# Kernel optimization log

Hardware: AMD Instinct MI355X
Metric: run time of the kernel (lower is better)

The kernel has to match this reference:

```python
import jax, jax.numpy as jnp
from jax import lax
import numpy as np

B, T, D, H = 2048, 512, 16, 48


def _lstm_layer(x, W_ih, W_hh, b_ih, b_hh):
    """Single-layer LSTM, batch_first. x: [B,T,Din] -> hs: [B,T,H].
    PyTorch gate order: i, f, g, o."""
    h_dim = W_hh.shape[1]
    # Precompute input contribution for all timesteps: [B,T,4H]
    xg = jnp.einsum('btd,gd->btg', x, W_ih) + b_ih + b_hh
    xg = jnp.swapaxes(xg, 0, 1)  # [T,B,4H]

    def step(carry, xg_t):
        h, c = carry
        gates = xg_t + h @ W_hh.T  # [B,4H]
        i, f, g, o = jnp.split(gates, 4, axis=-1)
        i = jax.nn.sigmoid(i)
        f = jax.nn.sigmoid(f)
        g = jnp.tanh(g)
        o = jax.nn.sigmoid(o)
        c = f * c + i * g
        h = o * jnp.tanh(c)
        return (h, c), h

    bsz = x.shape[0]
    init = (jnp.zeros((bsz, h_dim), x.dtype), jnp.zeros((bsz, h_dim), x.dtype))
    _, hs = lax.scan(step, init, xg)
    return jnp.swapaxes(hs, 0, 1)  # [B,T,H]


def setup_inputs() -> dict:
    key = jax.random.key(0)
    ks = jax.random.split(key, 11)
    s_in = 1.0 / np.sqrt(H)
    return {
        'x': jax.random.normal(ks[0], (B, T, D), jnp.float32),
        'W_ih0': jax.random.normal(ks[1], (4 * H, D), jnp.float32) * s_in,
        'W_hh0': jax.random.normal(ks[2], (4 * H, H), jnp.float32) * s_in,
        'b_ih0': jax.random.normal(ks[3], (4 * H,), jnp.float32) * s_in,
        'b_hh0': jax.random.normal(ks[4], (4 * H,), jnp.float32) * s_in,
        'W_ih1': jax.random.normal(ks[5], (4 * H, H), jnp.float32) * s_in,
        'W_hh1': jax.random.normal(ks[6], (4 * H, H), jnp.float32) * s_in,
        'b_ih1': jax.random.normal(ks[7], (4 * H,), jnp.float32) * s_in,
        'b_hh1': jax.random.normal(ks[8], (4 * H,), jnp.float32) * s_in,
        'fc_w': jax.random.normal(ks[9], (1, H), jnp.float32) * s_in,
        'fc_b': jax.random.normal(ks[10], (1,), jnp.float32) * s_in,
    }


def reference(x, W_ih0, W_hh0, b_ih0, b_hh0, W_ih1, W_hh1, b_ih1, b_hh1, fc_w, fc_b):
    # 2-layer LSTM (eval mode: inter-layer dropout is identity)
    h1 = _lstm_layer(x, W_ih0, W_hh0, b_ih0, b_hh0)   # [B,T,H]
    h2 = _lstm_layer(h1, W_ih1, W_hh1, b_ih1, b_hh1)  # [B,T,H]
    last = h2[:, -1, :]                               # [B,H]
    logits = last @ fc_w.T + fc_b                     # [B,1]
    return jax.nn.sigmoid(logits)
```

## Files before the change

kernel.cpp:

```cpp
#include <hip/hip_runtime.h>

#define TT 512
#define DD 16
#define HH 48
#define BT 8
#define NTHR 768
#define CHUNK 64

#define XA0H 16384
#define XA1  17920
#define STOT 20992

typedef short bf8v __attribute__((ext_vector_type(8)));
typedef float f32x4 __attribute__((ext_vector_type(4)));

__device__ __forceinline__ ushort bfb(float f) {
    return __builtin_bit_cast(ushort, (__bf16)f);
}

__device__ __forceinline__ float actf(float x, float A, float M, float Bc) {
    float e = __builtin_amdgcn_exp2f(M * x);
    return __builtin_fmaf(A, __builtin_amdgcn_rcpf(1.0f + e), Bc);
}

__device__ __forceinline__ void barrier_lds() {
    asm volatile("s_waitcnt lgkmcnt(0)\ns_barrier" ::: "memory");
}

__global__ __launch_bounds__(NTHR)
void lstm_kernel(const float* __restrict__ x,
                 const float* __restrict__ Wih0, const float* __restrict__ Whh0,
                 const float* __restrict__ bih0, const float* __restrict__ bhh0,
                 const float* __restrict__ Wih1, const float* __restrict__ Whh1,
                 const float* __restrict__ bih1, const float* __restrict__ bhh1,
                 const float* __restrict__ fcw, const float* __restrict__ fcb,
                 float* __restrict__ out)
{
    __shared__ alignas(16) ushort S[STOT];
    __shared__ float outl[BT][HH];

    const int tid  = threadIdx.x;
    const int lane = tid & 63;
    const int wave = tid >> 6;
    const int b0   = blockIdx.x * BT;

    const int colq = lane & 15;
    const int quad = lane >> 4;
    const int u    = wave * 4 + quad;
    const bool lo  = (colq < 8);

    const float L2E = 1.4426950408889634f;

    const int fb = colq * 8;
    const int inc01 = (quad < 2) ? 2 * 256 : 0;
    const int a1e = XA0H + (2 + quad) * 128 + fb;
    const int a1o = a1e + 768;
    const int g0e = XA1 + 1536 + quad * 128 + fb;
    const int g0o = g0e - 1536;
    const int w0  = (u >> 3) * 128 + fb + (u & 7);
    const int wA0e = XA0H + 768 + w0;
    const int wA0o = XA0H + w0;
    const int wr = lo ? ((u >> 3) * 128 + (colq + 8) * 8 + (u & 7))
                      : (((48 + u) >> 3) * 128 + colq * 8 + ((48 + u) & 7));
    const int wA1e = XA1 + wr;
    const int wA1o = XA1 + 1536 + wr;

    f32x4 bias0, bias1;
#pragma unroll
    for (int r = 0; r < 4; ++r) {
        bias0[r] = bih0[r * 48 + u] + bhh0[r * 48 + u];
        bias1[r] = bih1[r * 48 + u] + bhh1[r * 48 + u];
    }

    const int gi = (colq & 3) * 48 + wave * 4 + (colq >> 2);
    bf8v w0f0, w0f1, w1f0, w1f1, w1f2;
    {
        bf8v w;
#pragma unroll
        for (int j = 0; j < 8; ++j) {
            int k = quad * 8 + j;
            float v = (k < 16) ? Wih0[gi * 16 + k] : Whh0[gi * 48 + (k - 16)];
            w[j] = (short)bfb(v);
        }
        w0f0 = w;
#pragma unroll
        for (int j = 0; j < 8; ++j) {
            int k = 32 + quad * 8 + j;
            w[j] = (short)bfb(Whh0[gi * 48 + (k - 16)]);
        }
        w0f1 = w;
#pragma unroll
        for (int j = 0; j < 8; ++j) {
            int k = quad * 8 + j;
            w[j] = (short)bfb(Wih1[gi * 48 + k]);
        }
        w1f0 = w;
#pragma unroll
        for (int j = 0; j < 8; ++j) {
            int k = 32 + quad * 8 + j;
            float v = (k < 48) ? Wih1[gi * 48 + k] : Whh1[gi * 48 + (k - 48)];
            w[j] = (short)bfb(v);
        }
        w1f1 = w;
#pragma unroll
        for (int j = 0; j < 8; ++j) {
            int k = 64 + quad * 8 + j;
            w[j] = (short)bfb(Whh1[gi * 48 + (k - 48)]);
        }
        w1f2 = w;
    }

    {
        uint* p = (uint*)S;
        for (int i = tid; i < STOT / 2; i += NTHR) p[i] = 0;
    }
    __syncthreads();

    float c = 0.f;
    float hv = 0.f;

#define BODY(A0OFF, A1OFF, G0OFF, WA0OFF, WA1OFF, DOL1) { \
        bf8v a0 = *(const bf8v*)&S[A0OFF]; \
        bf8v a1 = *(const bf8v*)&S[A1OFF]; \
        f32x4 acc0 = __builtin_amdgcn_mfma_f32_16x16x32_bf16(w0f0, a0, bias0, 0, 0, 0); \
        acc0 = __builtin_amdgcn_mfma_f32_16x16x32_bf16(w0f1, a1, acc0, 0, 0, 0); \
        f32x4 pre; \
        if (DOL1) { \
            bf8v g0 = *(const bf8v*)&S[G0OFF]; \
            bf8v g1 = *(const bf8v*)&S[(G0OFF) + 512]; \
            bf8v g2 = *(const bf8v*)&S[(G0OFF) + 1024]; \
            f32x4 acc1 = __builtin_amdgcn_mfma_f32_16x16x32_bf16(w1f0, g0, bias1, 0, 0, 0); \
            acc1 = __builtin_amdgcn_mfma_f32_16x16x32_bf16(w1f1, g1, acc1, 0, 0, 0); \
            acc1 = __builtin_amdgcn_mfma_f32_16x16x32_bf16(w1f2, g2, acc1, 0, 0, 0); \
            pre[0] = lo ? acc0[0] : acc1[0]; \
            pre[1] = lo ? acc0[1] : acc1[1]; \
            pre[2] = lo ? acc0[2] : acc1[2]; \
            pre[3] = lo ? acc0[3] : acc1[3]; \
        } else { \
            pre = acc0; \
        } \
        float iv = actf(pre[0], 1.0f, -L2E, 0.0f); \
        float fv = actf(pre[1], 1.0f, -L2E, 0.0f); \
        float gv = actf(pre[2], 2.0f, -2.0f * L2E, -1.0f); \
        float ov = actf(pre[3], 1.0f, -L2E, 0.0f); \
        float cn = __builtin_fmaf(fv, c, iv * gv); \
        if (!DOL1) cn = lo ? cn : c;    \
        c = cn; \
        float tc = actf(cn, 2.0f, -2.0f * L2E, -1.0f); \
        hv = ov * tc; \
        ushort hb = bfb(hv); \
        if (DOL1) { S[WA1OFF] = hb; } \
        else if (lo) { S[WA1OFF] = hb; } \
        if (lo) S[WA0OFF] = hb; \
        barrier_lds(); \
    }

    for (int ck = 0; ck < TT / CHUNK; ++ck) {
        for (int i = tid; i < BT * CHUNK * 4; i += NTHR) {
            int g  = i & 3;
            int tl = (i >> 2) & (CHUNK - 1);
            int b  = i >> 8;
            const float4 v = *(const float4*)(x +
                ((size_t)(b0 + b) * TT + (ck * CHUNK + tl)) * DD + g * 4);
            ushort4 s4;
            s4.x = bfb(v.x); s4.y = bfb(v.y); s4.z = bfb(v.z); s4.w = bfb(v.w);
            *(ushort4*)&S[tl * 256 + (g >> 1) * 128 + b * 8 + (g & 1) * 4] = s4;
        }
        __syncthreads();

        int ae = (quad < 2) ? (quad * 128 + fb) : (XA0H + (quad - 2) * 128 + fb);
        int ao = (quad < 2) ? (256 + quad * 128 + fb) : (XA0H + 768 + (quad - 2) * 128 + fb);

        int p0 = 0;
        if (ck == 0) {
            BODY(ae, a1e, g0e, wA0e, wA1e, false)
            BODY(ao, a1o, g0o, wA0o, wA1o, true)
            ae += inc01; ao += inc01;
            p0 = 1;
        }
        for (int p = p0; p < CHUNK / 2; ++p) {
            BODY(ae, a1e, g0e, wA0e, wA1e, true)
            BODY(ao, a1o, g0o, wA0o, wA1o, true)
            ae += inc01; ao += inc01;
        }
    }

    {
        bf8v g0 = *(const bf8v*)&S[g0e];
        bf8v g1 = *(const bf8v*)&S[g0e + 512];
        bf8v g2 = *(const bf8v*)&S[g0e + 1024];
        f32x4 acc1 = __builtin_amdgcn_mfma_f32_16x16x32_bf16(w1f0, g0, bias1, 0, 0, 0);
        acc1 = __builtin_amdgcn_mfma_f32_16x16x32_bf16(w1f1, g1, acc1, 0, 0, 0);
        acc1 = __builtin_amdgcn_mfma_f32_16x16x32_bf16(w1f2, g2, acc1, 0, 0, 0);
        float iv = actf(acc1[0], 1.0f, -L2E, 0.0f);
        float fv = actf(acc1[1], 1.0f, -L2E, 0.0f);
        float gv = actf(acc1[2], 2.0f, -2.0f * L2E, -1.0f);
        float ov = actf(acc1[3], 1.0f, -L2E, 0.0f);
        float cn = __builtin_fmaf(fv, c, iv * gv);
        float tc = actf(cn, 2.0f, -2.0f * L2E, -1.0f);
        hv = ov * tc;
    }

    if (!lo) outl[colq - 8][u] = hv;
    __syncthreads();
    if (tid < BT) {
        float s = fcb[0];
        for (int uu = 0; uu < HH; ++uu) s = __builtin_fmaf(outl[tid][uu], fcw[uu], s);
        out[b0 + tid] = actf(s, 1.0f, -L2E, 0.0f);
    }
#undef BODY
}

extern "C" void kernel_launch(void* const* d_in, const int* in_sizes, int n_in,
                              void* d_out, int out_size, void* d_ws, size_t ws_size,
                              hipStream_t stream) {
    const float* x    = (const float*)d_in[0];
    const float* Wih0 = (const float*)d_in[1];
    const float* Whh0 = (const float*)d_in[2];
    const float* bih0 = (const float*)d_in[3];
    const float* bhh0 = (const float*)d_in[4];
    const float* Wih1 = (const float*)d_in[5];
    const float* Whh1 = (const float*)d_in[6];
    const float* bih1 = (const float*)d_in[7];
    const float* bhh1 = (const float*)d_in[8];
    const float* fcw  = (const float*)d_in[9];
    const float* fcb  = (const float*)d_in[10];
    lstm_kernel<<<2048 / BT, NTHR, 0, stream>>>(x, Wih0, Whh0, bih0, bhh0,
                                                Wih1, Whh1, bih1, bhh1, fcw, fcb,
                                                (float*)d_out);
}
```

Before: 307.7 us.

## Halve batch tile per block and give each wave two unit groups

Cuts the batch tile from 8 to 4 sequences per block and the block size from 768 to 384 threads. Each wave now computes two groups of hidden units with separate weight fragments, and the MFMA column layout is remapped so one 16-column tile packs both layers for the 4 batch rows. LDS layout and offsets are reorganised to match. The aim is twice as many blocks and cheaper per-step barriers across fewer waves, at the cost of twice the MFMAs per wave per step, more weight registers, and half-empty MFMA columns per sequence.

```diff
diff --git a/kernel.cpp b/kernel.cpp
--- a/kernel.cpp
+++ b/kernel.cpp
@@ -3,13 +3,12 @@
 #define TT 512
 #define DD 16
 #define HH 48
-#define BT 8
-#define NTHR 768
+#define BT 4
+#define NTHR 384
 #define CHUNK 64
 
-#define XA0H 16384
-#define XA1  17920
-#define STOT 20992
+#define XB 8192
+#define STOT 9728
 
 typedef short bf8v __attribute__((ext_vector_type(8)));
 typedef float f32x4 __attribute__((ext_vector_type(4)));
@@ -46,68 +45,76 @@
 
     const int colq = lane & 15;
     const int quad = lane >> 4;
-    const int u    = wave * 4 + quad;
-    const bool lo  = (colq < 8);
+    const int bcol = colq & 3;
+    const int isL1 = (colq >> 2) & 1;
+    const int u    = 8 * wave + ((colq & 8) ? 4 : 0) + quad;
+    const int uA   = 8 * wave + quad;
+    const int uB   = uA + 4;
 
     const float L2E = 1.4426950408889634f;
 
-    const int fb = colq * 8;
-    const int inc01 = (quad < 2) ? 2 * 256 : 0;
-    const int a1e = XA0H + (2 + quad) * 128 + fb;
-    const int a1o = a1e + 768;
-    const int g0e = XA1 + 1536 + quad * 128 + fb;
-    const int g0o = g0e - 1536;
-    const int w0  = (u >> 3) * 128 + fb + (u & 7);
-    const int wA0e = XA0H + 768 + w0;
-    const int wA0o = XA0H + w0;
-    const int wr = lo ? ((u >> 3) * 128 + (colq + 8) * 8 + (u & 7))
-                      : (((48 + u) >> 3) * 128 + colq * 8 + ((48 + u) & 7));
-    const int wA1e = XA1 + wr;
-    const int wA1o = XA1 + 1536 + wr;
-
-    f32x4 bias0, bias1;
+    const int fb = (colq & 7) * 8;
+    const int GE = XB + quad * 64 + fb;
+    const int GO = GE + 768;
+    const int inc = (quad < 2) ? 256 : 0;
+    const int o1 = ((16 + u) >> 3) * 64 + bcol * 8 + ((16 + u) & 7);
+    const int o2 = (u >> 3) * 64 + (4 + bcol) * 8 + (u & 7);
+    const int o3 = ((48 + u) >> 3) * 64 + (4 + bcol) * 8 + ((48 + u) & 7);
+
+    f32x4 b0A, b1A, b0B, b1B;
 #pragma unroll
     for (int r = 0; r < 4; ++r) {
-        bias0[r] = bih0[r * 48 + u] + bhh0[r * 48 + u];
-        bias1[r] = bih1[r * 48 + u] + bhh1[r * 48 + u];
-    }
-
-    const int gi = (colq & 3) * 48 + wave * 4 + (colq >> 2);
-    bf8v w0f0, w0f1, w1f0, w1f1, w1f2;
+        b0A[r] = bih0[r * 48 + uA] + bhh0[r * 48 + uA];
+        b1A[r] = bih1[r * 48 + uA] + bhh1[r * 48 + uA];
+        b0B[r] = bih0[r * 48 + uB] + bhh0[r * 48 + uB];
+        b1B[r] = bih1[r * 48 + uB] + bhh1[r * 48 + uB];
+    }
+
+    const int giA = (colq & 3) * 48 + 8 * wave + (colq >> 2);
+    const int giB = giA + 4;
+    bf8v wA0f0, wA0f1, wA1f0, wA1f1, wA1f2;
+    bf8v wB0f0, wB0f1, wB1f0, wB1f1, wB1f2;
     {
-        bf8v w;
-#pragma unroll
-        for (int j = 0; j < 8; ++j) {
-            int k = quad * 8 + j;
-            float v = (k < 16) ? Wih0[gi * 16 + k] : Whh0[gi * 48 + (k - 16)];
-            w[j] = (short)bfb(v);
-        }
-        w0f0 = w;
-#pragma unroll
-        for (int j = 0; j < 8; ++j) {
-            int k = 32 + quad * 8 + j;
-            w[j] = (short)bfb(Whh0[gi * 48 + (k - 16)]);
-        }
-        w0f1 = w;
-#pragma unroll
-        for (int j = 0; j < 8; ++j) {
-            int k = quad * 8 + j;
-            w[j] = (short)bfb(Wih1[gi * 48 + k]);
-        }
-        w1f0 = w;
-#pragma unroll
-        for (int j = 0; j < 8; ++j) {
-            int k = 32 + quad * 8 + j;
-            float v = (k < 48) ? Wih1[gi * 48 + k] : Whh1[gi * 48 + (k - 48)];
-            w[j] = (short)bfb(v);
-        }
-        w1f1 = w;
-#pragma unroll
-        for (int j = 0; j < 8; ++j) {
-            int k = 64 + quad * 8 + j;
-            w[j] = (short)bfb(Whh1[gi * 48 + (k - 48)]);
-        }
-        w1f2 = w;
+        auto l0 = [&](int gi, bf8v& f0, bf8v& f1) {
+            bf8v w;
+#pragma unroll
+            for (int j = 0; j < 8; ++j) {
+                int k = quad * 8 + j;
+                float v = (k < 16) ? Wih0[gi * 16 + k] : Whh0[gi * 48 + (k - 16)];
+                w[j] = (short)bfb(v);
+            }
+            f0 = w;
+#pragma unroll
+            for (int j = 0; j < 8; ++j) {
+                int k = 32 + quad * 8 + j;
+                w[j] = (short)bfb(Whh0[gi * 48 + (k - 16)]);
+            }
+            f1 = w;
+        };
+        auto l1 = [&](int gi, bf8v& f0, bf8v& f1, bf8v& f2) {
+            bf8v w;
+#pragma unroll
+            for (int j = 0; j < 8; ++j) {
+                int k = quad * 8 + j;
+                w[j] = (short)bfb(Wih1[gi * 48 + k]);
+            }
+            f0 = w;
+#pragma unroll
+            for (int j = 0; j < 8; ++j) {
+                int k = 32 + quad * 8 + j;
+                float v = (k < 48) ? Wih1[gi * 48 + k] : Whh1[gi * 48 + (k - 48)];
+                w[j] = (short)bfb(v);
+            }
+            f1 = w;
+#pragma unroll
+            for (int j = 0; j < 8; ++j) {
+                int k = 64 + quad * 8 + j;
+                w[j] = (short)bfb(Whh1[gi * 48 + (k - 48)]);
+            }
+            f2 = w;
+        };
+        l0(giA, wA0f0, wA0f1);  l1(giA, wA1f0, wA1f1, wA1f2);
+        l0(giB, wB0f0, wB0f1);  l1(giB, wB1f0, wB1f1, wB1f2);
     }
 
     {
@@ -119,39 +126,49 @@
     float c = 0.f;
     float hv = 0.f;
 
-#define BODY(A0OFF, A1OFF, G0OFF, WA0OFF, WA1OFF, DOL1) { \
+#define MFMA(A, B, C) __builtin_amdgcn_mfma_f32_16x16x32_bf16(A, B, C, 0, 0, 0)
+
+#define BODY(A0OFF, G0OFF, WBASE, DOL1) { \
         bf8v a0 = *(const bf8v*)&S[A0OFF]; \
-        bf8v a1 = *(const bf8v*)&S[A1OFF]; \
-        f32x4 acc0 = __builtin_amdgcn_mfma_f32_16x16x32_bf16(w0f0, a0, bias0, 0, 0, 0); \
-        acc0 = __builtin_amdgcn_mfma_f32_16x16x32_bf16(w0f1, a1, acc0, 0, 0, 0); \
-        f32x4 pre; \
+        bf8v g0 = *(const bf8v*)&S[G0OFF]; \
+        bf8v g1 = *(const bf8v*)&S[(G0OFF) + 256]; \
+        bf8v g2 = *(const bf8v*)&S[(G0OFF) + 512]; \
+        f32x4 a0A = MFMA(wA0f0, a0, b0A);  a0A = MFMA(wA0f1, g1, a0A); \
+        f32x4 a0B = MFMA(wB0f0, a0, b0B);  a0B = MFMA(wB0f1, g1, a0B); \
+        f32x4 sL0, pre; \
+        sL0[0] = (colq & 8) ? a0B[0] : a0A[0]; \
+        sL0[1] = (colq & 8) ? a0B[1] : a0A[1]; \
+        sL0[2] = (colq & 8) ? a0B[2] : a0A[2]; \
+        sL0[3] = (colq & 8) ? a0B[3] : a0A[3]; \
         if (DOL1) { \
-            bf8v g0 = *(const bf8v*)&S[G0OFF]; \
-            bf8v g1 = *(const bf8v*)&S[(G0OFF) + 512]; \
-            bf8v g2 = *(const bf8v*)&S[(G0OFF) + 1024]; \
-            f32x4 acc1 = __builtin_amdgcn_mfma_f32_16x16x32_bf16(w1f0, g0, bias1, 0, 0, 0); \
-            acc1 = __builtin_amdgcn_mfma_f32_16x16x32_bf16(w1f1, g1, acc1, 0, 0, 0); \
-            acc1 = __builtin_amdgcn_mfma_f32_16x16x32_bf16(w1f2, g2, acc1, 0, 0, 0); \
-            pre[0] = lo ? acc0[0] : acc1[0]; \
-            pre[1] = lo ? acc0[1] : acc1[1]; \
-            pre[2] = lo ? acc0[2] : acc1[2]; \
-            pre[3] = lo ? acc0[3] : acc1[3]; \
+            f32x4 a1A = MFMA(wA1f0, g0, b1A); \
+            a1A = MFMA(wA1f1, g1, a1A);  a1A = MFMA(wA1f2, g2, a1A); \
+            f32x4 a1B = MFMA(wB1f0, g0, b1B); \
+            a1B = MFMA(wB1f1, g1, a1B);  a1B = MFMA(wB1f2, g2, a1B); \
+            f32x4 sL1; \
+            sL1[0] = (colq & 8) ? a1B[0] : a1A[0]; \
+            sL1[1] = (colq & 8) ? a1B[1] : a1A[1]; \
+            sL1[2] = (colq & 8) ? a1B[2] : a1A[2]; \
+            sL1[3] = (colq & 8) ? a1B[3] : a1A[3]; \
+            pre[0] = isL1 ? sL1[0] : sL0[0]; \
+            pre[1] = isL1 ? sL1[1] : sL0[1]; \
+            pre[2] = isL1 ? sL1[2] : sL0[2]; \
+            pre[3] = isL1 ? sL1[3] : sL0[3]; \
         } else { \
-            pre = acc0; \
+            pre = sL0; \
         } \
         float iv = actf(pre[0], 1.0f, -L2E, 0.0f); \
         float fv = actf(pre[1], 1.0f, -L2E, 0.0f); \
         float gv = actf(pre[2], 2.0f, -2.0f * L2E, -1.0f); \
         float ov = actf(pre[3], 1.0f, -L2E, 0.0f); \
         float cn = __builtin_fmaf(fv, c, iv * gv); \
-        if (!DOL1) cn = lo ? cn : c;    \
+        if (!DOL1) cn = isL1 ? c : cn;    \
         c = cn; \
         float tc = actf(cn, 2.0f, -2.0f * L2E, -1.0f); \
         hv = ov * tc; \
         ushort hb = bfb(hv); \
-        if (DOL1) { S[WA1OFF] = hb; } \
-        else if (lo) { S[WA1OFF] = hb; } \
-        if (lo) S[WA0OFF] = hb; \
+        if (!isL1) { S[(WBASE) + o1] = hb; S[(WBASE) + o2] = hb; } \
+        else if (DOL1) { S[(WBASE) + o3] = hb; } \
         barrier_lds(); \
     }
 
@@ -164,44 +181,50 @@
                 ((size_t)(b0 + b) * TT + (ck * CHUNK + tl)) * DD + g * 4);
             ushort4 s4;
             s4.x = bfb(v.x); s4.y = bfb(v.y); s4.z = bfb(v.z); s4.w = bfb(v.w);
-            *(ushort4*)&S[tl * 256 + (g >> 1) * 128 + b * 8 + (g & 1) * 4] = s4;
+            *(ushort4*)&S[tl * 128 + (g >> 1) * 64 + b * 8 + (g & 1) * 4] = s4;
         }
         __syncthreads();
 
-        int ae = (quad < 2) ? (quad * 128 + fb) : (XA0H + (quad - 2) * 128 + fb);
-        int ao = (quad < 2) ? (256 + quad * 128 + fb) : (XA0H + 768 + (quad - 2) * 128 + fb);
+        int aE = (quad < 2) ? (quad * 64 + fb) : (XB + quad * 64 + fb);
+        int aO = (quad < 2) ? (128 + quad * 64 + fb) : (XB + 768 + quad * 64 + fb);
 
         int p0 = 0;
         if (ck == 0) {
-            BODY(ae, a1e, g0e, wA0e, wA1e, false)
-            BODY(ao, a1o, g0o, wA0o, wA1o, true)
-            ae += inc01; ao += inc01;
+            BODY(aE, GE, XB + 768, false)
+            BODY(aO, GO, XB, true)
+            aE += inc; aO += inc;
             p0 = 1;
         }
         for (int p = p0; p < CHUNK / 2; ++p) {
-            BODY(ae, a1e, g0e, wA0e, wA1e, true)
-            BODY(ao, a1o, g0o, wA0o, wA1o, true)
-            ae += inc01; ao += inc01;
+            BODY(aE, GE, XB + 768, true)
+            BODY(aO, GO, XB, true)
+            aE += inc; aO += inc;
         }
     }
 
     {
-        bf8v g0 = *(const bf8v*)&S[g0e];
-        bf8v g1 = *(const bf8v*)&S[g0e + 512];
-        bf8v g2 = *(const bf8v*)&S[g0e + 1024];
-        f32x4 acc1 = __builtin_amdgcn_mfma_f32_16x16x32_bf16(w1f0, g0, bias1, 0, 0, 0);
-        acc1 = __builtin_amdgcn_mfma_f32_16x16x32_bf16(w1f1, g1, acc1, 0, 0, 0);
-        acc1 = __builtin_amdgcn_mfma_f32_16x16x32_bf16(w1f2, g2, acc1, 0, 0, 0);
-        float iv = actf(acc1[0], 1.0f, -L2E, 0.0f);
-        float fv = actf(acc1[1], 1.0f, -L2E, 0.0f);
-        float gv = actf(acc1[2], 2.0f, -2.0f * L2E, -1.0f);
-        float ov = actf(acc1[3], 1.0f, -L2E, 0.0f);
+        bf8v g0 = *(const bf8v*)&S[GE];
+        bf8v g1 = *(const bf8v*)&S[GE + 256];
+        bf8v g2 = *(const bf8v*)&S[GE + 512];
+        f32x4 a1A = MFMA(wA1f0, g0, b1A);
+        a1A = MFMA(wA1f1, g1, a1A);  a1A = MFMA(wA1f2, g2, a1A);
+        f32x4 a1B = MFMA(wB1f0, g0, b1B);
+        a1B = MFMA(wB1f1, g1, a1B);  a1B = MFMA(wB1f2, g2, a1B);
+        f32x4 sL1;
+        sL1[0] = (colq & 8) ? a1B[0] : a1A[0];
+        sL1[1] = (colq & 8) ? a1B[1] : a1A[1];
+        sL1[2] = (colq & 8) ? a1B[2] : a1A[2];
+        sL1[3] = (colq & 8) ? a1B[3] : a1A[3];
+        float iv = actf(sL1[0], 1.0f, -L2E, 0.0f);
+        float fv = actf(sL1[1], 1.0f, -L2E, 0.0f);
+        float gv = actf(sL1[2], 2.0f, -2.0f * L2E, -1.0f);
+        float ov = actf(sL1[3], 1.0f, -L2E, 0.0f);
         float cn = __builtin_fmaf(fv, c, iv * gv);
         float tc = actf(cn, 2.0f, -2.0f * L2E, -1.0f);
         hv = ov * tc;
     }
 
-    if (!lo) outl[colq - 8][u] = hv;
+    if (isL1) outl[bcol][u] = hv;
     __syncthreads();
     if (tid < BT) {
         float s = fcb[0];
@@ -209,6 +232,7 @@
         out[b0 + tid] = actf(s, 1.0f, -L2E, 0.0f);
     }
 #undef BODY
+#undef MFMA
 }
 
 extern "C" void kernel_launch(void* const* d_in, const int* in_sizes, int n_in,
```

Measured after the change: 491.9 us. 59.9% more time.

## Share B-operand fragments between both LSTM layers via unified LDS h-buffer layout

Applied to the files above, without the earlier changes.

Reorders the packed K dimension so that layer-0 (h0, x) and layer-1 (h1 input, h2) MFMAs read the same three LDS fragments, cutting per-step LDS reads from five to three. Each lane now writes its hidden state once to a single shared buffer, and the x staging area is halved in size using a 64-wide row layout. This reduces LDS traffic and footprint on the serial recurrence path, at the cost of more intricate index arithmetic that must stay correct for the ring/static split.

```diff
diff --git a/kernel.cpp b/kernel.cpp
--- a/kernel.cpp
+++ b/kernel.cpp
@@ -7,9 +7,8 @@
 #define NTHR 768
 #define CHUNK 64
 
-#define XA0H 16384
-#define XA1  17920
-#define STOT 20992
+#define XB 8192
+#define STOT (XB + 1536)
 
 typedef short bf8v __attribute__((ext_vector_type(8)));
 typedef float f32x4 __attribute__((ext_vector_type(4)));
@@ -46,24 +45,26 @@
 
     const int colq = lane & 15;
     const int quad = lane >> 4;
+    const int b    = colq & 7;
+    const bool hi  = (colq >= 8);
     const int u    = wave * 4 + quad;
-    const bool lo  = (colq < 8);
 
     const float L2E = 1.4426950408889634f;
 
-    const int fb = colq * 8;
-    const int inc01 = (quad < 2) ? 2 * 256 : 0;
-    const int a1e = XA0H + (2 + quad) * 128 + fb;
-    const int a1o = a1e + 768;
-    const int g0e = XA1 + 1536 + quad * 128 + fb;
-    const int g0o = g0e - 1536;
-    const int w0  = (u >> 3) * 128 + fb + (u & 7);
-    const int wA0e = XA0H + 768 + w0;
-    const int wA0o = XA0H + w0;
-    const int wr = lo ? ((u >> 3) * 128 + (colq + 8) * 8 + (u & 7))
-                      : (((48 + u) >> 3) * 128 + colq * 8 + ((48 + u) & 7));
-    const int wA1e = XA1 + wr;
-    const int wA1o = XA1 + 1536 + wr;
+    const int fbm = b * 8;
+    const bool ringlane = (quad >= 2) && !hi;
+    const int r0E = XB + quad * 64 + fbm;
+    const int r0O = r0E + 768;
+    const int r2E = XB + (8 + quad) * 64 + fbm;
+    const int r2O = r2E + 768;
+    const int r1statE = XB + (4 + quad) * 64 + fbm;
+    const int r1statO = r1statE + 768;
+    const int r1ring0 = (quad - 2) * 64 + colq * 8;
+    const int inc = ringlane ? 256 : 0;
+    const int kk = hi ? 48 + u : u;
+    const int woff = (kk >> 3) * 64 + b * 8 + (kk & 7);
+    const int wE = XB + 768 + woff;
+    const int wO = XB + woff;
 
     f32x4 bias0, bias1;
 #pragma unroll
@@ -73,41 +74,41 @@
     }
 
     const int gi = (colq & 3) * 48 + wave * 4 + (colq >> 2);
-    bf8v w0f0, w0f1, w1f0, w1f1, w1f2;
+    bf8v w0k0, w0k1, w1k0, w1k1, w1k2;
     {
         bf8v w;
 #pragma unroll
         for (int j = 0; j < 8; ++j) {
             int k = quad * 8 + j;
-            float v = (k < 16) ? Wih0[gi * 16 + k] : Whh0[gi * 48 + (k - 16)];
+            w[j] = (short)bfb(Whh0[gi * 48 + k]);
+        }
+        w0k0 = w;
+#pragma unroll
+        for (int j = 0; j < 8; ++j) {
+            int k = 32 + quad * 8 + j;
+            float v = (k < 48) ? Whh0[gi * 48 + k] : Wih0[gi * 16 + (k - 48)];
             w[j] = (short)bfb(v);
         }
-        w0f0 = w;
-#pragma unroll
-        for (int j = 0; j < 8; ++j) {
-            int k = 32 + quad * 8 + j;
-            w[j] = (short)bfb(Whh0[gi * 48 + (k - 16)]);
-        }
-        w0f1 = w;
+        w0k1 = w;
 #pragma unroll
         for (int j = 0; j < 8; ++j) {
             int k = quad * 8 + j;
             w[j] = (short)bfb(Wih1[gi * 48 + k]);
         }
-        w1f0 = w;
+        w1k0 = w;
 #pragma unroll
         for (int j = 0; j < 8; ++j) {
             int k = 32 + quad * 8 + j;
             float v = (k < 48) ? Wih1[gi * 48 + k] : Whh1[gi * 48 + (k - 48)];
             w[j] = (short)bfb(v);
         }
-        w1f1 = w;
+        w1k1 = w;
 #pragma unroll
         for (int j = 0; j < 8; ++j) {
             int k = 64 + quad * 8 + j;
             w[j] = (short)bfb(Whh1[gi * 48 + (k - 48)]);
         }
-        w1f2 = w;
+        w1k2 = w;
     }
 
     {
@@ -119,23 +120,23 @@
     float c = 0.f;
     float hv = 0.f;
 
-#define BODY(A0OFF, A1OFF, G0OFF, WA0OFF, WA1OFF, DOL1) { \
-        bf8v a0 = *(const bf8v*)&S[A0OFF]; \
-        bf8v a1 = *(const bf8v*)&S[A1OFF]; \
-        f32x4 acc0 = __builtin_amdgcn_mfma_f32_16x16x32_bf16(w0f0, a0, bias0, 0, 0, 0); \
-        acc0 = __builtin_amdgcn_mfma_f32_16x16x32_bf16(w0f1, a1, acc0, 0, 0, 0); \
+#define MFMA(A, B, C) __builtin_amdgcn_mfma_f32_16x16x32_bf16(A, B, C, 0, 0, 0)
+
+#define BODY(V0A, V1A, V2A, WA, DOL1) { \
+        bf8v v0 = *(const bf8v*)&S[V0A]; \
+        bf8v v1 = *(const bf8v*)&S[V1A]; \
+        bf8v v2 = *(const bf8v*)&S[V2A]; \
+        f32x4 acc0 = MFMA(w0k0, v0, bias0); \
+        acc0 = MFMA(w0k1, v1, acc0); \
         f32x4 pre; \
         if (DOL1) { \
-            bf8v g0 = *(const bf8v*)&S[G0OFF]; \
-            bf8v g1 = *(const bf8v*)&S[(G0OFF) + 512]; \
-            bf8v g2 = *(const bf8v*)&S[(G0OFF) + 1024]; \
-            f32x4 acc1 = __builtin_amdgcn_mfma_f32_16x16x32_bf16(w1f0, g0, bias1, 0, 0, 0); \
-            acc1 = __builtin_amdgcn_mfma_f32_16x16x32_bf16(w1f1, g1, acc1, 0, 0, 0); \
-            acc1 = __builtin_amdgcn_mfma_f32_16x16x32_bf16(w1f2, g2, acc1, 0, 0, 0); \
-            pre[0] = lo ? acc0[0] : acc1[0]; \
-            pre[1] = lo ? acc0[1] : acc1[1]; \
-            pre[2] = lo ? acc0[2] : acc1[2]; \
-            pre[3] = lo ? acc0[3] : acc1[3]; \
+            f32x4 acc1 = MFMA(w1k0, v0, bias1); \
+            acc1 = MFMA(w1k1, v1, acc1); \
+            acc1 = MFMA(w1k2, v2, acc1); \
+            pre[0] = hi ? acc1[0] : acc0[0]; \
+            pre[1] = hi ? acc1[1] : acc0[1]; \
+            pre[2] = hi ? acc1[2] : acc0[2]; \
+            pre[3] = hi ? acc1[3] : acc0[3]; \
         } else { \
             pre = acc0; \
         } \
@@ -144,14 +145,13 @@
         float gv = actf(pre[2], 2.0f, -2.0f * L2E, -1.0f); \
         float ov = actf(pre[3], 1.0f, -L2E, 0.0f); \
         float cn = __builtin_fmaf(fv, c, iv * gv); \
-        if (!DOL1) cn = lo ? cn : c;    \
+        if (!DOL1) cn = hi ? c : cn;    \
         c = cn; \
         float tc = actf(cn, 2.0f, -2.0f * L2E, -1.0f); \
         hv = ov * tc; \
         ushort hb = bfb(hv); \
-        if (DOL1) { S[WA1OFF] = hb; } \
-        else if (lo) { S[WA1OFF] = hb; } \
-        if (lo) S[WA0OFF] = hb; \
+        if (!hi) { S[WA] = hb; } \
+        else if (DOL1) { S[WA] = hb; } \
         barrier_lds(); \
     }
 
@@ -159,39 +159,40 @@
         for (int i = tid; i < BT * CHUNK * 4; i += NTHR) {
             int g  = i & 3;
             int tl = (i >> 2) & (CHUNK - 1);
-            int b  = i >> 8;
+            int bb = i >> 8;
             const float4 v = *(const float4*)(x +
-                ((size_t)(b0 + b) * TT + (ck * CHUNK + tl)) * DD + g * 4);
+                ((size_t)(b0 + bb) * TT + (ck * CHUNK + tl)) * DD + g * 4);
             ushort4 s4;
             s4.x = bfb(v.x); s4.y = bfb(v.y); s4.z = bfb(v.z); s4.w = bfb(v.w);
-            *(ushort4*)&S[tl * 256 + (g >> 1) * 128 + b * 8 + (g & 1) * 4] = s4;
+            *(ushort4*)&S[tl * 128 + (g >> 1) * 64 + bb * 8 + (g & 1) * 4] = s4;
         }
         __syncthreads();
 
-        int ae = (quad < 2) ? (quad * 128 + fb) : (XA0H + (quad - 2) * 128 + fb);
-        int ao = (quad < 2) ? (256 + quad * 128 + fb) : (XA0H + 768 + (quad - 2) * 128 + fb);
+        int r1E = ringlane ? r1ring0 : r1statE;
+        int r1O = ringlane ? (128 + r1ring0) : r1statO;
 
         int p0 = 0;
         if (ck == 0) {
-            BODY(ae, a1e, g0e, wA0e, wA1e, false)
-            BODY(ao, a1o, g0o, wA0o, wA1o, true)
-            ae += inc01; ao += inc01;
+            BODY(r0E, r1E, r2E, wE, false)
+            BODY(r0O, r1O, r2O, wO, true)
+            r1E += inc; r1O += inc;
             p0 = 1;
         }
         for (int p = p0; p < CHUNK / 2; ++p) {
-            BODY(ae, a1e, g0e, wA0e, wA1e, true)
-            BODY(ao, a1o, g0o, wA0o, wA1o, true)
-            ae += inc01; ao += inc01;
+            BODY(r0E, r1E, r2E, wE, true)
+            BODY(r0O, r1O, r2O, wO, true)
+            r1E += inc; r1O += inc;
         }
     }
 
     {
-        bf8v g0 = *(const bf8v*)&S[g0e];
-        bf8v g1 = *(const bf8v*)&S[g0e + 512];
-        bf8v g2 = *(const bf8v*)&S[g0e + 1024];
-        f32x4 acc1 = __builtin_amdgcn_mfma_f32_16x16x32_bf16(w1f0, g0, bias1, 0, 0, 0);
-        acc1 = __builtin_amdgcn_mfma_f32_16x16x32_bf16(w1f1, g1, acc1, 0, 0, 0);
-        acc1 = __builtin_amdgcn_mfma_f32_16x16x32_bf16(w1f2, g2, acc1, 0, 0, 0);
+        int r1E = ringlane ? (r1ring0 + 32 * 256) : r1statE;
+        bf8v v0 = *(const bf8v*)&S[r0E];
+        bf8v v1 = *(const bf8v*)&S[r1E];
+        bf8v v2 = *(const bf8v*)&S[r2E];
+        f32x4 acc1 = MFMA(w1k0, v0, bias1);
+        acc1 = MFMA(w1k1, v1, acc1);
+        acc1 = MFMA(w1k2, v2, acc1);
         float iv = actf(acc1[0], 1.0f, -L2E, 0.0f);
         float fv = actf(acc1[1], 1.0f, -L2E, 0.0f);
         float gv = actf(acc1[2], 2.0f, -2.0f * L2E, -1.0f);
@@ -201,7 +202,7 @@
         hv = ov * tc;
     }
 
-    if (!lo) outl[colq - 8][u] = hv;
+    if (hi) outl[b][u] = hv;
     __syncthreads();
     if (tid < BT) {
         float s = fcb[0];
@@ -209,6 +210,7 @@
         out[b0 + tid] = actf(s, 1.0f, -L2E, 0.0f);
     }
 #undef BODY
+#undef MFMA
 }
 
 extern "C" void kernel_launch(void* const* d_in, const int* in_sizes, int n_in,
```

Result: faster. 295.3 us (-4.0%).
